# Optimization experiments

Hardware: AMD Instinct MI355X
Metric: run time of the kernel (lower is better)

The kernel has to match this reference:

```python
import jax, jax.numpy as jnp
import numpy as np

N = 6144          # atoms (~300 residues)
K = 6             # sequence-separation bins (k_vals clamped to 0..5)
T = 85            # RASP 'all' atom types
D = 21            # distance bins -> max_d = 20 A
NBRE_NT_EXCLU = 2 # exclude pairs with residue separation <= 2
N_RES = 307


def setup_inputs() -> dict:
    key = jax.random.key(0)
    k1, k2, k3, k4, k5 = jax.random.split(key, 5)
    # coords scaled so pair distances populate the 0..20 A bin range
    coords = jax.random.normal(k1, (N, 3), jnp.float32) * 5.0
    # atoms grouped by residue -> sorted residue ids
    res_ids = jnp.sort(jax.random.randint(k2, (N,), 0, N_RES)).astype(jnp.int32)
    types = jax.random.randint(k3, (N,), 0, T).astype(jnp.int32)
    types = jnp.where(jax.random.uniform(k4, (N,)) < 0.02, jnp.int32(-1), types)
    pot_tensor = jax.random.normal(k5, (K, T, T, D), jnp.float32) * 0.5
    return {"coords": coords, "res_ids": res_ids, "types": types, "pot_tensor": pot_tensor}


def reference(coords, res_ids, types, pot_tensor):
    n = coords.shape[0]
    # static upper-triangular pair indices (i < j), as in torch.triu_indices(offset=1)
    ii_np, jj_np = np.triu_indices(n, k=1)
    ii = jnp.asarray(ii_np, jnp.int32)
    jj = jnp.asarray(jj_np, jnp.int32)

    sep = jnp.abs(res_ids[ii] - res_ids[jj])                       # [P]
    mask = (sep > NBRE_NT_EXCLU) & (types[ii] != -1) & (types[jj] != -1)

    diff = coords[ii] - coords[jj]                                 # [P,3]
    dists = jnp.sqrt(jnp.sum(diff * diff, axis=1)) + 1e-8          # [P]

    k_vals = jnp.clip(sep - 1, 0, 5)
    max_d = pot_tensor.shape[3] - 1
    d0 = jnp.floor(jnp.clip(dists, 0, max_d)).astype(jnp.int32)
    d1 = jnp.minimum(d0 + 1, max_d)
    alpha = dists - d0.astype(dists.dtype)

    # masked pairs may carry type -1; redirect their gather to index 0
    # (their contribution is zeroed by `mask` below, matching torch semantics)
    ti = jnp.where(mask, types[ii], 0)
    tj = jnp.where(mask, types[jj], 0)

    e0 = pot_tensor[k_vals, ti, tj, d0]                            # [P] 4D gather
    e1 = pot_tensor[k_vals, ti, tj, d1]

    contrib = ((1.0 - alpha) * e0 + alpha * e1 - 2.7)
    contrib = contrib * (dists < max_d).astype(contrib.dtype) * mask.astype(contrib.dtype)
    return jnp.sum(contrib)
```

## Files before the change

kernel.cpp:

```cpp
#include <hip/hip_runtime.h>


#define T_TYPES 85
#define D_BINS 21
#define TSTRIDE (T_TYPES * D_BINS)
#define KSTRIDE (T_TYPES * T_TYPES * D_BINS)
#define INVALID_KEY 85
#define NKEYS 86
#define TILE 128
#define PTHREADS 512
#define JCHUNK (TILE / (PTHREADS / TILE))
#define MAXSLOTS 36

__global__ __launch_bounds__(1024) void sort_kernel(const float* __restrict__ coords,
                                                    const int* __restrict__ res_ids,
                                                    const int* __restrict__ types, int n,
                                                    float4* __restrict__ sorted,
                                                    float* __restrict__ out) {
    __shared__ int hist[NKEYS];
    __shared__ int offs[NKEYS];
    int tid = threadIdx.x;
    if (tid < NKEYS) hist[tid] = 0;
    if (tid == 0) *out = 0.0f;
    __syncthreads();
    for (int i = tid; i < n; i += 1024) {
        int t = types[i];
        atomicAdd(&hist[(t < 0) ? INVALID_KEY : t], 1);
    }
    __syncthreads();
    if (tid == 0) {
        int s = 0;
        for (int i = 0; i < NKEYS; ++i) { offs[i] = s; s += hist[i]; }
    }
    __syncthreads();
    for (int i = tid; i < n; i += 1024) {
        int t = types[i];
        int key = (t < 0) ? INVALID_KEY : t;
        int pos = atomicAdd(&offs[key], 1);
        float4 v;
        if (t < 0) {
            v.x = 1.0e6f + 1000.0f * (float)pos;
            v.y = 0.0f; v.z = 0.0f;
            v.w = __int_as_float((res_ids[i] << 7) | 84);
        } else {
            v.x = coords[3 * i + 0];
            v.y = coords[3 * i + 1];
            v.z = coords[3 * i + 2];
            v.w = __int_as_float((res_ids[i] << 7) | t);
        }
        sorted[pos] = v;
    }
}

__global__ __launch_bounds__(PTHREADS) void pair_kernel(const float4* __restrict__ sorted,
                                                        const float* __restrict__ pot,
                                                        int n, int nt,
                                                        float* __restrict__ out) {
    __shared__ float4 jtile[TILE];
    __shared__ float pot_s[6 * MAXSLOTS * D_BINS];
    __shared__ float wsum[PTHREADS / 64];

    int b = blockIdx.x;
    int bi = (int)((2.0 * nt + 1.0 -
                    sqrt((2.0 * nt + 1.0) * (2.0 * nt + 1.0) - 8.0 * (double)b)) * 0.5);
    if (bi < 0) bi = 0;
    if (bi > nt - 1) bi = nt - 1;
    while ((bi + 1) * nt - ((bi + 1) * bi) / 2 <= b) ++bi;
    while (bi * nt - (bi * (bi - 1)) / 2 > b) --bi;
    int bj = bi + (b - (bi * nt - (bi * (bi - 1)) / 2));

    int tid = threadIdx.x;
    int ilane = tid & (TILE - 1);
    int chunk = tid >> 7;
    int i0 = bi * TILE, q0 = bj * TILE;

    int ihi = min(i0 + TILE, n) - 1;
    int jhi = min(q0 + TILE, n) - 1;
    int tloi = min(__float_as_int(sorted[i0].w) & 127, 84);
    int thii = min(__float_as_int(sorted[ihi].w) & 127, 84);
    int tloj = min(__float_as_int(sorted[q0].w) & 127, 84);
    int thij = min(__float_as_int(sorted[jhi].w) & 127, 84);
    int nti = thii - tloi + 1;
    int ntj = thij - tloj + 1;
    int slots = nti * ntj;
    bool staged = (slots <= MAXSLOTS);

    if (tid < TILE) {
        int q = q0 + tid;
        float4 v;
        if (q < n) v = sorted[q];
        else { v.x = 3.0e7f; v.y = 0.f; v.z = 0.f; v.w = __int_as_float(0); }
        jtile[tid] = v;
    }

    if (staged) {
        int total = 6 * slots * D_BINS;
        for (int e = tid; e < total; e += PTHREADS) {
            int d = e % D_BINS;
            int s2 = e / D_BINS;
            int slot = s2 % slots;
            int k = s2 / slots;
            int tii = slot / ntj;
            int tjj = slot - tii * ntj;
            pot_s[e] = pot[k * KSTRIDE + (tloi + tii) * TSTRIDE + (tloj + tjj) * D_BINS + d];
        }
    }
    __syncthreads();

    int p = i0 + ilane;
    float4 mine;
    if (p < n) mine = sorted[p];
    else { mine.x = 2.0e7f; mine.y = 0.f; mine.z = 0.f; mine.w = __int_as_float(0); }

    int pki = __float_as_int(mine.w);
    int keyi = pki & 127;
    int resi = pki >> 7;
    int islot = min(max(keyi - tloi, 0), nti - 1);
    int sbase = islot * ntj;
    int tibase_g = min(keyi, 84) * TSTRIDE;
    int pjb = p - q0;

    float acc = 0.0f;
    int j0 = chunk * JCHUNK;

    if (staged) {
#pragma unroll 8
        for (int u = 0; u < JCHUNK; ++u) {
            int jj = j0 + u;
            float4 o = jtile[jj];
            float dx = mine.x - o.x;
            float dy = mine.y - o.y;
            float dz = mine.z - o.z;
            float d2 = dx * dx + dy * dy + dz * dz;
            float dist = __builtin_amdgcn_sqrtf(d2);

            int pkj = __float_as_int(o.w);
            int keyj = pkj & 127;
            int resj = pkj >> 7;
            int sep = abs(resi - resj);
            int jslot = min(max(keyj - tloj, 0), ntj - 1);
            int k = min(max(sep - 1, 0), 5);
            int d0i = min((int)dist, 19);
            float alpha = dist - (float)d0i;

            int li = (k * slots + sbase + jslot) * D_BINS + d0i;
            float e0 = pot_s[li];
            float e1 = pot_s[li + 1];
            float val = __builtin_fmaf(alpha, e1 - e0, e0) - 2.7f;
            bool valid = (sep > 2) && (dist < 20.0f) && (jj > pjb);
            acc += valid ? val : 0.0f;
        }
    } else {
#pragma unroll 4
        for (int u = 0; u < JCHUNK; ++u) {
            int jj = j0 + u;
            float4 o = jtile[jj];
            float dx = mine.x - o.x;
            float dy = mine.y - o.y;
            float dz = mine.z - o.z;
            float d2 = dx * dx + dy * dy + dz * dz;
            float dist = __builtin_amdgcn_sqrtf(d2);

            int pkj = __float_as_int(o.w);
            int keyj = min(pkj & 127, 84);
            int resj = pkj >> 7;
            int sep = abs(resi - resj);
            int k = min(max(sep - 1, 0), 5);
            int d0i = min((int)dist, 19);
            float alpha = dist - (float)d0i;

            int gi = k * KSTRIDE + tibase_g + keyj * D_BINS + d0i;
            float e0 = pot[gi];
            float e1 = pot[gi + 1];
            float val = __builtin_fmaf(alpha, e1 - e0, e0) - 2.7f;
            bool valid = (sep > 2) && (dist < 20.0f) && (jj > pjb);
            acc += valid ? val : 0.0f;
        }
    }

#pragma unroll
    for (int off = 32; off > 0; off >>= 1)
        acc += __shfl_down(acc, off, 64);
    int wave = tid >> 6;
    int lane = tid & 63;
    if (lane == 0) wsum[wave] = acc;
    __syncthreads();
    if (tid == 0) {
        float s = 0.f;
#pragma unroll
        for (int w = 0; w < PTHREADS / 64; ++w) s += wsum[w];
        atomicAdd(out, s);
    }
}

extern "C" void kernel_launch(void* const* d_in, const int* in_sizes, int n_in,
                              void* d_out, int out_size, void* d_ws, size_t ws_size,
                              hipStream_t stream) {
    const float* coords = (const float*)d_in[0];
    const int* res_ids = (const int*)d_in[1];
    const int* types   = (const int*)d_in[2];
    const float* pot   = (const float*)d_in[3];
    int n = in_sizes[1];
    float* out = (float*)d_out;

    float4* sorted = (float4*)d_ws;

    sort_kernel<<<1, 1024, 0, stream>>>(coords, res_ids, types, n, sorted, out);

    int nt = (n + TILE - 1) / TILE;
    int nblocks = nt * (nt + 1) / 2;
    pair_kernel<<<nblocks, PTHREADS, 0, stream>>>(sorted, pot, n, nt, out);
}
```

Baseline: 94.02 us.

## Broadcast j-atoms via readlane, two i-atoms per thread, split diagonal tiles

The pair kernel no longer stages the j tile in shared memory. Each wave holds 16 j atoms in registers and broadcasts them with readlane, while every thread processes two i atoms. This cuts LDS traffic and halves per-pair j-loading overhead. Diagonal and off-diagonal tiles now use separate template instantiations, so off-diagonal tiles skip the triangular check. The sort kernel also replaces its serial prefix sum with a parallel scan. The cost is higher register pressure from the fully unrolled loop over two atoms.

```diff
diff --git a/kernel.cpp b/kernel.cpp
--- a/kernel.cpp
+++ b/kernel.cpp
@@ -9,7 +9,6 @@
 #define NKEYS 86
 #define TILE 128
 #define PTHREADS 512
-#define JCHUNK (TILE / (PTHREADS / TILE))
 #define MAXSLOTS 36
 
 __global__ __launch_bounds__(1024) void sort_kernel(const float* __restrict__ coords,
@@ -18,6 +17,7 @@
                                                     float4* __restrict__ sorted,
                                                     float* __restrict__ out) {
     __shared__ int hist[NKEYS];
+    __shared__ int sc[NKEYS];
     __shared__ int offs[NKEYS];
     int tid = threadIdx.x;
     if (tid < NKEYS) hist[tid] = 0;
@@ -28,10 +28,17 @@
         atomicAdd(&hist[(t < 0) ? INVALID_KEY : t], 1);
     }
     __syncthreads();
-    if (tid == 0) {
-        int s = 0;
-        for (int i = 0; i < NKEYS; ++i) { offs[i] = s; s += hist[i]; }
-    }
+    if (tid < NKEYS) sc[tid] = hist[tid];
+    __syncthreads();
+#pragma unroll
+    for (int off = 1; off < NKEYS; off <<= 1) {
+        int v = 0;
+        if (tid < NKEYS && tid >= off) v = sc[tid - off];
+        __syncthreads();
+        if (tid < NKEYS) sc[tid] += v;
+        __syncthreads();
+    }
+    if (tid < NKEYS) offs[tid] = sc[tid] - hist[tid];
     __syncthreads();
     for (int i = tid; i < n; i += 1024) {
         int t = types[i];
@@ -52,11 +59,115 @@
     }
 }
 
+__device__ __forceinline__ float bcastf(float v, int u) {
+    return __int_as_float(__builtin_amdgcn_readlane(__float_as_int(v), u));
+}
+
+template <bool DIAG>
+__device__ __forceinline__ void pair_body(const float4& jreg, const float4& m0, const float4& m1,
+                                          const float* __restrict__ pot_s,
+                                          int resi0, int resi1, int sb21_0, int sb21_1,
+                                          int slots21, int tloj, int ntj,
+                                          int jbase, int p0, int p1,
+                                          float& acc0, float& acc1) {
+#pragma unroll
+    for (int u = 0; u < 16; ++u) {
+        float ox = bcastf(jreg.x, u);
+        float oy = bcastf(jreg.y, u);
+        float oz = bcastf(jreg.z, u);
+        int pw = __builtin_amdgcn_readlane(__float_as_int(jreg.w), u);
+        int keyj = pw & 127;
+        int resj = pw >> 7;
+        int jslot = min(max(keyj - tloj, 0), ntj - 1);
+        int jb = jslot * D_BINS;
+        int q = jbase + u;
+
+        {
+            float dx = m0.x - ox, dy = m0.y - oy, dz = m0.z - oz;
+            float d2 = dx * dx + dy * dy + dz * dz;
+            float dist = __builtin_amdgcn_sqrtf(d2);
+            int sep = abs(resi0 - resj);
+            int k = min(max(sep - 1, 0), 5);
+            int d0i = min((int)dist, 19);
+            float alpha = dist - (float)d0i;
+            int li = k * slots21 + sb21_0 + jb + d0i;
+            float e0 = pot_s[li];
+            float e1 = pot_s[li + 1];
+            float val = __builtin_fmaf(alpha, e1 - e0, e0) - 2.7f;
+            bool valid = (sep > 2) && (dist < 20.0f);
+            if (DIAG) valid = valid && (q > p0);
+            acc0 += valid ? val : 0.0f;
+        }
+        {
+            float dx = m1.x - ox, dy = m1.y - oy, dz = m1.z - oz;
+            float d2 = dx * dx + dy * dy + dz * dz;
+            float dist = __builtin_amdgcn_sqrtf(d2);
+            int sep = abs(resi1 - resj);
+            int k = min(max(sep - 1, 0), 5);
+            int d0i = min((int)dist, 19);
+            float alpha = dist - (float)d0i;
+            int li = k * slots21 + sb21_1 + jb + d0i;
+            float e0 = pot_s[li];
+            float e1 = pot_s[li + 1];
+            float val = __builtin_fmaf(alpha, e1 - e0, e0) - 2.7f;
+            bool valid = (sep > 2) && (dist < 20.0f);
+            if (DIAG) valid = valid && (q > p1);
+            acc1 += valid ? val : 0.0f;
+        }
+    }
+}
+
+template <bool DIAG>
+__device__ __forceinline__ void pair_body_global(const float4& jreg, const float4& m0, const float4& m1,
+                                                 const float* __restrict__ pot,
+                                                 int resi0, int resi1, int tib0, int tib1,
+                                                 int jbase, int p0, int p1,
+                                                 float& acc0, float& acc1) {
+#pragma unroll
+    for (int u = 0; u < 16; ++u) {
+        float ox = bcastf(jreg.x, u);
+        float oy = bcastf(jreg.y, u);
+        float oz = bcastf(jreg.z, u);
+        int pw = __builtin_amdgcn_readlane(__float_as_int(jreg.w), u);
+        int keyj = min(pw & 127, 84);
+        int resj = pw >> 7;
+        int jb = keyj * D_BINS;
+        int q = jbase + u;
+        {
+            float dx = m0.x - ox, dy = m0.y - oy, dz = m0.z - oz;
+            float dist = __builtin_amdgcn_sqrtf(dx * dx + dy * dy + dz * dz);
+            int sep = abs(resi0 - resj);
+            int k = min(max(sep - 1, 0), 5);
+            int d0i = min((int)dist, 19);
+            float alpha = dist - (float)d0i;
+            int gi = k * KSTRIDE + tib0 + jb + d0i;
+            float e0 = pot[gi], e1 = pot[gi + 1];
+            float val = __builtin_fmaf(alpha, e1 - e0, e0) - 2.7f;
+            bool valid = (sep > 2) && (dist < 20.0f);
+            if (DIAG) valid = valid && (q > p0);
+            acc0 += valid ? val : 0.0f;
+        }
+        {
+            float dx = m1.x - ox, dy = m1.y - oy, dz = m1.z - oz;
+            float dist = __builtin_amdgcn_sqrtf(dx * dx + dy * dy + dz * dz);
+            int sep = abs(resi1 - resj);
+            int k = min(max(sep - 1, 0), 5);
+            int d0i = min((int)dist, 19);
+            float alpha = dist - (float)d0i;
+            int gi = k * KSTRIDE + tib1 + jb + d0i;
+            float e0 = pot[gi], e1 = pot[gi + 1];
+            float val = __builtin_fmaf(alpha, e1 - e0, e0) - 2.7f;
+            bool valid = (sep > 2) && (dist < 20.0f);
+            if (DIAG) valid = valid && (q > p1);
+            acc1 += valid ? val : 0.0f;
+        }
+    }
+}
+
 __global__ __launch_bounds__(PTHREADS) void pair_kernel(const float4* __restrict__ sorted,
                                                         const float* __restrict__ pot,
                                                         int n, int nt,
                                                         float* __restrict__ out) {
-    __shared__ float4 jtile[TILE];
     __shared__ float pot_s[6 * MAXSLOTS * D_BINS];
     __shared__ float wsum[PTHREADS / 64];
 
@@ -70,8 +181,8 @@
     int bj = bi + (b - (bi * nt - (bi * (bi - 1)) / 2));
 
     int tid = threadIdx.x;
-    int ilane = tid & (TILE - 1);
-    int chunk = tid >> 7;
+    int lane = tid & 63;
+    int jc = tid >> 6;
     int i0 = bi * TILE, q0 = bj * TILE;
 
     int ihi = min(i0 + TILE, n) - 1;
@@ -83,18 +194,11 @@
     int nti = thii - tloi + 1;
     int ntj = thij - tloj + 1;
     int slots = nti * ntj;
+    int slots21 = slots * D_BINS;
     bool staged = (slots <= MAXSLOTS);
 
-    if (tid < TILE) {
-        int q = q0 + tid;
-        float4 v;
-        if (q < n) v = sorted[q];
-        else { v.x = 3.0e7f; v.y = 0.f; v.z = 0.f; v.w = __int_as_float(0); }
-        jtile[tid] = v;
-    }
-
     if (staged) {
-        int total = 6 * slots * D_BINS;
+        int total = 6 * slots21;
         for (int e = tid; e < total; e += PTHREADS) {
             int d = e % D_BINS;
             int s2 = e / D_BINS;
@@ -105,84 +209,55 @@
             pot_s[e] = pot[k * KSTRIDE + (tloi + tii) * TSTRIDE + (tloj + tjj) * D_BINS + d];
         }
     }
-    __syncthreads();
-
-    int p = i0 + ilane;
-    float4 mine;
-    if (p < n) mine = sorted[p];
-    else { mine.x = 2.0e7f; mine.y = 0.f; mine.z = 0.f; mine.w = __int_as_float(0); }
-
-    int pki = __float_as_int(mine.w);
-    int keyi = pki & 127;
-    int resi = pki >> 7;
-    int islot = min(max(keyi - tloi, 0), nti - 1);
-    int sbase = islot * ntj;
-    int tibase_g = min(keyi, 84) * TSTRIDE;
-    int pjb = p - q0;
-
-    float acc = 0.0f;
-    int j0 = chunk * JCHUNK;
-
+
+    int jbase = q0 + jc * 16;
+    int jl = jbase + (lane & 15);
+    float4 jreg;
+    if (jl < n) jreg = sorted[jl];
+    else { jreg.x = 3.0e7f; jreg.y = 0.f; jreg.z = 0.f; jreg.w = __int_as_float(84); }
+
+    int p0 = i0 + (lane);
+    int p1 = i0 + 64 + (lane);
+    float4 m0, m1;
+    if (p0 < n) m0 = sorted[p0];
+    else { m0.x = 2.0e7f; m0.y = 0.f; m0.z = 0.f; m0.w = __int_as_float(84); }
+    if (p1 < n) m1 = sorted[p1];
+    else { m1.x = 2.5e7f; m1.y = 0.f; m1.z = 0.f; m1.w = __int_as_float(84); }
+
+    int pk0 = __float_as_int(m0.w), pk1 = __float_as_int(m1.w);
+    int key0 = pk0 & 127, key1 = pk1 & 127;
+    int resi0 = pk0 >> 7, resi1 = pk1 >> 7;
+    int islot0 = min(max(key0 - tloi, 0), nti - 1);
+    int islot1 = min(max(key1 - tloi, 0), nti - 1);
+    int sb21_0 = islot0 * ntj * D_BINS;
+    int sb21_1 = islot1 * ntj * D_BINS;
+    int tib0 = min(key0, 84) * TSTRIDE;
+    int tib1 = min(key1, 84) * TSTRIDE;
+
+    __syncthreads();
+
+    float acc0 = 0.f, acc1 = 0.f;
     if (staged) {
-#pragma unroll 8
-        for (int u = 0; u < JCHUNK; ++u) {
-            int jj = j0 + u;
-            float4 o = jtile[jj];
-            float dx = mine.x - o.x;
-            float dy = mine.y - o.y;
-            float dz = mine.z - o.z;
-            float d2 = dx * dx + dy * dy + dz * dz;
-            float dist = __builtin_amdgcn_sqrtf(d2);
-
-            int pkj = __float_as_int(o.w);
-            int keyj = pkj & 127;
-            int resj = pkj >> 7;
-            int sep = abs(resi - resj);
-            int jslot = min(max(keyj - tloj, 0), ntj - 1);
-            int k = min(max(sep - 1, 0), 5);
-            int d0i = min((int)dist, 19);
-            float alpha = dist - (float)d0i;
-
-            int li = (k * slots + sbase + jslot) * D_BINS + d0i;
-            float e0 = pot_s[li];
-            float e1 = pot_s[li + 1];
-            float val = __builtin_fmaf(alpha, e1 - e0, e0) - 2.7f;
-            bool valid = (sep > 2) && (dist < 20.0f) && (jj > pjb);
-            acc += valid ? val : 0.0f;
-        }
+        if (bi == bj)
+            pair_body<true>(jreg, m0, m1, pot_s, resi0, resi1, sb21_0, sb21_1,
+                            slots21, tloj, ntj, jbase, p0, p1, acc0, acc1);
+        else
+            pair_body<false>(jreg, m0, m1, pot_s, resi0, resi1, sb21_0, sb21_1,
+                             slots21, tloj, ntj, jbase, p0, p1, acc0, acc1);
     } else {
-#pragma unroll 4
-        for (int u = 0; u < JCHUNK; ++u) {
-            int jj = j0 + u;
-            float4 o = jtile[jj];
-            float dx = mine.x - o.x;
-            float dy = mine.y - o.y;
-            float dz = mine.z - o.z;
-            float d2 = dx * dx + dy * dy + dz * dz;
-            float dist = __builtin_amdgcn_sqrtf(d2);
-
-            int pkj = __float_as_int(o.w);
-            int keyj = min(pkj & 127, 84);
-            int resj = pkj >> 7;
-            int sep = abs(resi - resj);
-            int k = min(max(sep - 1, 0), 5);
-            int d0i = min((int)dist, 19);
-            float alpha = dist - (float)d0i;
-
-            int gi = k * KSTRIDE + tibase_g + keyj * D_BINS + d0i;
-            float e0 = pot[gi];
-            float e1 = pot[gi + 1];
-            float val = __builtin_fmaf(alpha, e1 - e0, e0) - 2.7f;
-            bool valid = (sep > 2) && (dist < 20.0f) && (jj > pjb);
-            acc += valid ? val : 0.0f;
-        }
-    }
-
+        if (bi == bj)
+            pair_body_global<true>(jreg, m0, m1, pot, resi0, resi1, tib0, tib1,
+                                   jbase, p0, p1, acc0, acc1);
+        else
+            pair_body_global<false>(jreg, m0, m1, pot, resi0, resi1, tib0, tib1,
+                                    jbase, p0, p1, acc0, acc1);
+    }
+
+    float acc = acc0 + acc1;
 #pragma unroll
     for (int off = 32; off > 0; off >>= 1)
         acc += __shfl_down(acc, off, 64);
     int wave = tid >> 6;
-    int lane = tid & 63;
     if (lane == 0) wsum[wave] = acc;
     __syncthreads();
     if (tid == 0) {
```

After: 94.03 us. No clear change (+0.0%).
